# Kernel tuning notes

Measured on AMD Instinct MI355X. Metric: run time of the kernel, lower is better.

## Reference

```python
import jax, jax.numpy as jnp
import numpy as np

N_NODES = 200000
N_EDGES = 1600000
NUM_GRAPHS = 2000
VOCAB = 10000
D = 64
NUM_CLS = 2


def setup_inputs() -> dict:
    key = jax.random.key(0)
    ks = jax.random.split(key, 12)
    x = jax.random.randint(ks[0], (N_NODES,), 0, VOCAB, dtype=jnp.int32)
    edge_index = jax.random.randint(ks[1], (2, N_EDGES), 0, N_NODES, dtype=jnp.int32)
    edge_type = jax.random.randint(ks[2], (N_EDGES,), 0, 8, dtype=jnp.int32)
    batch = jnp.sort(jax.random.randint(ks[3], (N_NODES,), 0, NUM_GRAPHS, dtype=jnp.int32))
    embed_table = jax.random.normal(ks[4], (VOCAB, D), dtype=jnp.float32) * 0.02
    embed_table = embed_table.at[0].set(0.0)  # padding_idx=0
    W1 = jax.random.normal(ks[5], (D, D), dtype=jnp.float32) * (1.0 / np.sqrt(D))
    b1 = jnp.zeros((D,), dtype=jnp.float32)
    W2 = jax.random.normal(ks[6], (D, D), dtype=jnp.float32) * (1.0 / np.sqrt(D))
    b2 = jnp.zeros((D,), dtype=jnp.float32)
    Wlin = jax.random.normal(ks[7], (D, NUM_CLS), dtype=jnp.float32) * (1.0 / np.sqrt(D))
    blin = jnp.zeros((NUM_CLS,), dtype=jnp.float32)
    return {"x": x, "edge_index": edge_index, "edge_type": edge_type, "batch": batch,
            "embed_table": embed_table, "W1": W1, "b1": b1, "W2": W2, "b2": b2,
            "Wlin": Wlin, "blin": blin}


def reference(x, edge_index, edge_type, batch, embed_table, W1, b1, W2, b2, Wlin, blin):
    n = x.shape[0]
    # GCN normalization with self-loops (PyG GCNConv default, edge weight = 1)
    loops = jnp.arange(n, dtype=edge_index.dtype)
    src = jnp.concatenate([edge_index[0], loops])
    dst = jnp.concatenate([edge_index[1], loops])
    deg = jax.ops.segment_sum(jnp.ones_like(src, dtype=jnp.float32), dst, num_segments=n)
    dinv = jax.lax.rsqrt(deg)  # deg >= 1 due to self-loops
    norm = (dinv[src] * dinv[dst])[:, None]  # [E+N, 1]

    def gcn(h, W, b):
        h = h @ W  # transform first (small GEMM)
        agg = jax.ops.segment_sum(norm * h[src], dst, num_segments=n)
        return agg + b

    h = embed_table[x]                      # [N, D] embedding lookup
    h = jax.nn.relu(gcn(h, W1, b1))
    h = jax.nn.relu(gcn(h, W2, b2))
    # global mean pool over graphs
    sums = jax.ops.segment_sum(h, batch, num_segments=NUM_GRAPHS)
    cnts = jax.ops.segment_sum(jnp.ones((n,), dtype=h.dtype), batch, num_segments=NUM_GRAPHS)
    g = sums / jnp.maximum(cnts, 1.0)[:, None]
    return g @ Wlin + blin
```

## Files before the change

### kernel.cpp

```cpp
#include <hip/hip_runtime.h>
#include <hip/hip_fp16.h>


#define DD 64
#define BKT 256
#define MAXK 1024
#define NBLK 256
#define BTE 1024
#define SRCMASK 0x3FFFF
#define PBUF_CAP 4096
#define PCAP 4096
#define CCAP 4880
#define CHCAP 6656

typedef _Float16 half8_t __attribute__((ext_vector_type(8)));
typedef float float4_t __attribute__((ext_vector_type(4)));
union F4H8 { float4 f; half8_t h; };
union H8   { float4 f; __half2 h[4]; };

static __device__ __forceinline__ void atomAddF(float* p, float v) {
    unsafeAtomicAdd(p, v);
}

__global__ __launch_bounds__(256) void prep_kernel(
        const float2* __restrict__ table2, __half2* __restrict__ th2, int n2,
        const float* __restrict__ W1, const float* __restrict__ W2,
        __half* __restrict__ w1t, __half* __restrict__ w2t,
        float* __restrict__ outacc, int G2, int* __restrict__ bcur, int K) {
    int gid = blockIdx.x * 256 + threadIdx.x;
    int stride = gridDim.x * 256;
    for (int i = gid; i < K; i += stride) bcur[i] = i * PCAP;
    for (int i = gid; i < G2; i += stride) outacc[i] = 0.f;
    for (int i = gid; i < n2; i += stride)
        th2[i] = __float22half2_rn(table2[i]);
    for (int i = gid; i < DD * DD; i += stride) {
        int n = i >> 6, k = i & 63;
        w1t[i] = __float2half(W1[k * DD + n]);
        w2t[i] = __float2half(W2[k * DD + n]);
    }
}

__global__ __launch_bounds__(BTE) void fused_fill_kernel(
        const int* __restrict__ src, const int* __restrict__ dst, int E, int CH,
        int* __restrict__ bcur, int* __restrict__ pairbuf, int K) {
    __shared__ int lh[MAXK];
    __shared__ int lpk[CHCAP];
    __shared__ unsigned short lbk[CHCAP];
    int tid = threadIdx.x;
    for (int i = tid; i < K; i += BTE) lh[i] = 0;
    __syncthreads();
    int e0 = blockIdx.x * CH;
    int e1 = min(E, e0 + CH);
    int L = e1 - e0;
    bool fits = (L <= CHCAP);
    if (fits) {
        for (int i = tid; i < L; i += BTE) {
            int s = src[e0 + i], d = dst[e0 + i];
            unsigned b = ((unsigned)d) >> 8;
            lpk[i] = s | ((d & 255) << 24);
            lbk[i] = (unsigned short)b;
            atomicAdd(&lh[b], 1);
        }
    } else {
        for (int e = e0 + tid; e < e1; e += BTE)
            atomicAdd(&lh[((unsigned)dst[e]) >> 8], 1);
    }
    __syncthreads();
    for (int b = tid; b < K; b += BTE) {
        int c = lh[b];
        lh[b] = (c > 0) ? atomicAdd(&bcur[b], c) : 0;
    }
    __syncthreads();
    if (fits) {
        for (int i = tid; i < L; i += BTE) {
            int pos = atomicAdd(&lh[lbk[i]], 1);
            pairbuf[pos] = lpk[i];
        }
    } else {
        for (int e = e0 + tid; e < e1; e += BTE) {
            int s = src[e], d = dst[e];
            int pos = atomicAdd(&lh[((unsigned)d) >> 8], 1);
            pairbuf[pos] = s | ((d & 255) << 24);
        }
    }
}

__global__ __launch_bounds__(256) void build_csr_kernel(
        const int* __restrict__ pairbuf, const int* __restrict__ bcur,
        const int* __restrict__ x, int2* __restrict__ rowinfo,
        float2* __restrict__ xd, __half* __restrict__ dinvh,
        int* __restrict__ csr_src, __half* __restrict__ g1h, int N) {
    __shared__ int cnt[256], basel[256], curl[256];
    __shared__ int pbuf[PBUF_CAP];
    int tid = threadIdx.x;
    int b = blockIdx.x;
    int node0 = b << 8;
    cnt[tid] = 0;
    __syncthreads();
    int bb0 = b * PCAP;
    int L   = bcur[b] - bb0;
    bool fits = (L <= PBUF_CAP);
    if (fits) {
        for (int i = tid; i < L; i += 256) {
            int pk = pairbuf[bb0 + i];
            pbuf[i] = pk;
            atomicAdd(&cnt[((unsigned)pk) >> 24], 1);
        }
    } else {
        for (int i = tid; i < L; i += 256)
            atomicAdd(&cnt[((unsigned)pairbuf[bb0 + i]) >> 24], 1);
    }
    __syncthreads();
    int c  = cnt[tid];
    int pc = (c + 3) & ~3;
    {
        __syncthreads();
        basel[tid] = pc;
        __syncthreads();
        if (tid < 64) {
            int carry = 0;
            for (int cc = 0; cc < 4; ++cc) {
                int orig = basel[cc * 64 + tid];
                int v = orig;
                #pragma unroll
                for (int off = 1; off < 64; off <<= 1) {
                    int t = __shfl_up(v, off);
                    if (tid >= off) v += t;
                }
                int tot = __shfl(v, 63);
                cnt[cc * 64 + tid] = v - orig + carry;
                carry += tot;
            }
        }
        __syncthreads();
    }
    int cb0 = b * CCAP;
    int node = node0 + tid;
    int myBase = cb0 + cnt[tid];
    curl[tid] = myBase;
    if (node < N) {
        rowinfo[node] = make_int2(myBase, pc);
        float di = rsqrtf((float)c + 1.0f);
        xd[node] = make_float2(di, __int_as_float(x[node]));
        dinvh[node] = __float2half(di);
        for (int t = c; t < pc; ++t) csr_src[myBase + t] = N;
    } else if (node == N) {
        xd[N] = make_float2(0.0f, __int_as_float(0));
        dinvh[N] = __float2half(0.0f);
        float2* z = (float2*)(g1h + (size_t)N * DD);
        for (int t = 0; t < DD / 4; ++t) z[t] = make_float2(0.f, 0.f);
    }
    __syncthreads();
    if (fits) {
        for (int i = tid; i < L; i += 256) {
            int pk = pbuf[i];
            int pos = atomicAdd(&curl[((unsigned)pk) >> 24], 1);
            int s = pk & 0x00FFFFFF;
            csr_src[pos] = (int)(((unsigned)s) | (((unsigned)x[s]) << 18));
        }
    } else {
        for (int i = tid; i < L; i += 256) {
            int pk = pairbuf[bb0 + i];
            int pos = atomicAdd(&curl[((unsigned)pk) >> 24], 1);
            int s = pk & 0x00FFFFFF;
            csr_src[pos] = (int)(((unsigned)s) | (((unsigned)x[s]) << 18));
        }
    }
}

#define L1_BODY4(sA)                                                          \
    do {                                                                      \
        unsigned a0 = (unsigned)(sA).x, a1 = (unsigned)(sA).y;                \
        unsigned a2 = (unsigned)(sA).z, a3 = (unsigned)(sA).w;                \
        H8 u0, u1, u2, u3;                                                    \
        u0.f = th4[(size_t)(a0 >> 18) * 8 + j3];                              \
        u1.f = th4[(size_t)(a1 >> 18) * 8 + j3];                              \
        u2.f = th4[(size_t)(a2 >> 18) * 8 + j3];                              \
        u3.f = th4[(size_t)(a3 >> 18) * 8 + j3];                              \
        __half2 w0 = __half2half2(dinvh[a0 & SRCMASK]);                       \
        __half2 w1 = __half2half2(dinvh[a1 & SRCMASK]);                       \
        __half2 w2 = __half2half2(dinvh[a2 & SRCMASK]);                       \
        __half2 w3 = __half2half2(dinvh[a3 & SRCMASK]);                       \
        _Pragma("unroll")                                                     \
        for (int t = 0; t < 4; ++t) {                                         \
            acc0.h[t] = __hfma2(w0, u0.h[t], acc0.h[t]);                      \
            acc1.h[t] = __hfma2(w1, u1.h[t], acc1.h[t]);                      \
            acc2.h[t] = __hfma2(w2, u2.h[t], acc2.h[t]);                      \
            acc3.h[t] = __hfma2(w3, u3.h[t], acc3.h[t]);                      \
        }                                                                     \
    } while (0)

__global__ __launch_bounds__(256, 8) void layer1_kernel(
        const int2* __restrict__ rowinfo,
        const int* __restrict__ csr_src, const float2* __restrict__ xd,
        const __half* __restrict__ dinvh,
        const float4* __restrict__ th4, const __half* __restrict__ wt,
        const float* __restrict__ bias, __half* __restrict__ g1h, int N) {
    __shared__ float4 Hs4[32 * 9];
    __shared__ float dvs[32];
    int row0 = blockIdx.x * 32;
    int tid = threadIdx.x;
    int node_l = tid >> 3, j3 = tid & 7;
    int node = row0 + node_l;
    H8 acc0, acc1, acc2, acc3;
    acc0.f = make_float4(0.f, 0.f, 0.f, 0.f);
    acc1.f = acc0.f; acc2.f = acc0.f; acc3.f = acc0.f;
    __half2 dh = __float2half2_rn(0.f);
    if (node < N) {
        float2 sxd = xd[node];
        float di = sxd.x;
        if (j3 == 0) dvs[node_l] = di;
        dh = __float2half2_rn(di);
        int2 ri = rowinfo[node];
        const int4* cs = (const int4*)(csr_src + ri.x);
        int nq = ri.y >> 2;
        int4 c0 = {0, 0, 0, 0}, c1 = c0, c2 = c0, c3 = c0;
        if (nq > 0) c0 = cs[0];
        if (nq > 1) c1 = cs[1];
        if (nq > 2) c2 = cs[2];
        if (nq > 3) c3 = cs[3];
        H8 tv; tv.f = th4[(size_t)__float_as_int(sxd.y) * 8 + j3];
        acc0.h[0] = __hmul2(dh, tv.h[0]); acc0.h[1] = __hmul2(dh, tv.h[1]);
        acc0.h[2] = __hmul2(dh, tv.h[2]); acc0.h[3] = __hmul2(dh, tv.h[3]);
        if (nq > 0) L1_BODY4(c0);
        if (nq > 1) L1_BODY4(c1);
        if (nq > 2) L1_BODY4(c2);
        if (nq > 3) L1_BODY4(c3);
        for (int q = 4; q < nq; ++q) {
            int4 cq = cs[q];
            L1_BODY4(cq);
        }
        #pragma unroll
        for (int t = 0; t < 4; ++t)
            acc0.h[t] = __hmul2(dh, __hadd2(__hadd2(acc0.h[t], acc1.h[t]),
                                            __hadd2(acc2.h[t], acc3.h[t])));
    }
    Hs4[node_l * 9 + j3] = acc0.f;
    __syncthreads();

    int wave = tid >> 6, lane = tid & 63;
    int m = lane & 15, quad = lane >> 4;
    int ncol = wave * 16 + m;
    F4H8 b0, b1;
    const float4* WT4 = (const float4*)wt;
    b0.f = WT4[ncol * 8 + quad];
    b1.f = WT4[ncol * 8 + 4 + quad];
    float bb_ = bias[ncol];
    #pragma unroll
    for (int t = 0; t < 2; ++t) {
        F4H8 a0, a1;
        a0.f = Hs4[(t * 16 + m) * 9 + quad];
        a1.f = Hs4[(t * 16 + m) * 9 + 4 + quad];
        float4_t acc = {0.f, 0.f, 0.f, 0.f};
        acc = __builtin_amdgcn_mfma_f32_16x16x32_f16(a0.h, b0.h, acc, 0, 0, 0);
        acc = __builtin_amdgcn_mfma_f32_16x16x32_f16(a1.h, b1.h, acc, 0, 0, 0);
        #pragma unroll
        for (int reg = 0; reg < 4; ++reg) {
            int row = t * 16 + quad * 4 + reg;
            int grow = row0 + row;
            if (grow < N) {
                float h = fmaxf(acc[reg] + bb_, 0.0f);
                g1h[(size_t)grow * DD + ncol] = __float2half(dvs[row] * h);
            }
        }
    }
}

#define L2_BODY4(sA)                                                          \
    do {                                                                      \
        H8 u0, u1, u2, u3;                                                    \
        u0.f = g1h4[(size_t)((sA).x & SRCMASK) * 8 + j3];                     \
        u1.f = g1h4[(size_t)((sA).y & SRCMASK) * 8 + j3];                     \
        u2.f = g1h4[(size_t)((sA).z & SRCMASK) * 8 + j3];                     \
        u3.f = g1h4[(size_t)((sA).w & SRCMASK) * 8 + j3];                     \
        _Pragma("unroll")                                                     \
        for (int t = 0; t < 4; ++t) {                                         \
            acc0.h[t] = __hadd2(acc0.h[t], u0.h[t]);                          \
            acc1.h[t] = __hadd2(acc1.h[t], u1.h[t]);                          \
            acc2.h[t] = __hadd2(acc2.h[t], u2.h[t]);                          \
            acc3.h[t] = __hadd2(acc3.h[t], u3.h[t]);                          \
        }                                                                     \
    } while (0)

__global__ __launch_bounds__(256, 8) void layer2_pool_kernel(
        const int2* __restrict__ rowinfo,
        const int* __restrict__ csr_src, const float2* __restrict__ xd,
        const float4* __restrict__ g1h4, const __half* __restrict__ wt,
        const float* __restrict__ bias, const int* __restrict__ batch,
        const float* __restrict__ Wlin, float* __restrict__ outacc, int N) {
    __shared__ float4 Hs4[32 * 9];
    __shared__ float lp0[128], lp1[128];
    __shared__ float p0s[32], p1s[32];
    __shared__ int   bat[32];
    int row0 = blockIdx.x * 32;
    int tid = threadIdx.x;
    int node_l = tid >> 3, j3 = tid & 7;
    int node = row0 + node_l;
    H8 acc0, acc1, acc2, acc3;
    acc0.f = make_float4(0.f, 0.f, 0.f, 0.f);
    acc1.f = acc0.f; acc2.f = acc0.f; acc3.f = acc0.f;
    if (node < N) {
        float di = xd[node].x;
        int2 ri = rowinfo[node];
        const int4* cs = (const int4*)(csr_src + ri.x);
        int nq = ri.y >> 2;
        int4 c0 = {0, 0, 0, 0}, c1 = c0, c2 = c0, c3 = c0;
        if (nq > 0) c0 = cs[0];
        if (nq > 1) c1 = cs[1];
        if (nq > 2) c2 = cs[2];
        if (nq > 3) c3 = cs[3];
        acc0.f = g1h4[(size_t)node * 8 + j3];
        if (nq > 0) L2_BODY4(c0);
        if (nq > 1) L2_BODY4(c1);
        if (nq > 2) L2_BODY4(c2);
        if (nq > 3) L2_BODY4(c3);
        for (int q = 4; q < nq; ++q) {
            int4 cq = cs[q];
            L2_BODY4(cq);
        }
        __half2 dih = __float2half2_rn(di);
        #pragma unroll
        for (int t = 0; t < 4; ++t)
            acc0.h[t] = __hmul2(dih, __hadd2(__hadd2(acc0.h[t], acc1.h[t]),
                                             __hadd2(acc2.h[t], acc3.h[t])));
    }
    Hs4[node_l * 9 + j3] = acc0.f;
    __syncthreads();

    int wave = tid >> 6, lane = tid & 63;
    int m = lane & 15, quad = lane >> 4;
    int ncol = wave * 16 + m;
    F4H8 b0, b1;
    const float4* WT4 = (const float4*)wt;
    b0.f = WT4[ncol * 8 + quad];
    b1.f = WT4[ncol * 8 + 4 + quad];
    float bb_  = bias[ncol];
    float wl0 = Wlin[ncol * 2 + 0];
    float wl1 = Wlin[ncol * 2 + 1];
    #pragma unroll
    for (int t = 0; t < 2; ++t) {
        F4H8 a0, a1;
        a0.f = Hs4[(t * 16 + m) * 9 + quad];
        a1.f = Hs4[(t * 16 + m) * 9 + 4 + quad];
        float4_t acc = {0.f, 0.f, 0.f, 0.f};
        acc = __builtin_amdgcn_mfma_f32_16x16x32_f16(a0.h, b0.h, acc, 0, 0, 0);
        acc = __builtin_amdgcn_mfma_f32_16x16x32_f16(a1.h, b1.h, acc, 0, 0, 0);
        #pragma unroll
        for (int reg = 0; reg < 4; ++reg) {
            int row = t * 16 + quad * 4 + reg;
            int grow = row0 + row;
            float h = (grow < N) ? fmaxf(acc[reg] + bb_, 0.0f) : 0.0f;
            float p0 = h * wl0;
            float p1 = h * wl1;
            #pragma unroll
            for (int off = 8; off >= 1; off >>= 1) {
                p0 += __shfl_xor(p0, off);
                p1 += __shfl_xor(p1, off);
            }
            if (m == 0) {
                lp0[wave * 32 + row] = p0;
                lp1[wave * 32 + row] = p1;
            }
        }
    }
    __syncthreads();
    if (tid < 32) {
        int grow = row0 + tid;
        p0s[tid] = lp0[tid] + lp0[32 + tid] + lp0[64 + tid] + lp0[96 + tid];
        p1s[tid] = lp1[tid] + lp1[32 + tid] + lp1[64 + tid] + lp1[96 + tid];
        bat[tid] = (grow < N) ? batch[grow] : -1;
    }
    __syncthreads();
    if (tid < 32) {
        float s0 = p0s[tid], s1 = p1s[tid];
        int bg = bat[tid];
        #pragma unroll
        for (int off = 1; off < 32; off <<= 1) {
            float t0 = __shfl_down(s0, off);
            float t1 = __shfl_down(s1, off);
            if (tid + off < 32 && bat[tid + off] == bg) {
                s0 += t0;
                s1 += t1;
            }
        }
        bool head = (bg >= 0) && (tid == 0 || bat[tid - 1] != bg);
        if (head) {
            atomAddF(&outacc[bg * 2 + 0], s0);
            atomAddF(&outacc[bg * 2 + 1], s1);
        }
    }
}

__global__ void final_kernel(const float* __restrict__ outacc,
                             const int* __restrict__ batch,
                             const float* __restrict__ blin,
                             float* __restrict__ out, int G, int N) {
    int t = blockIdx.x * blockDim.x + threadIdx.x;
    if (t >= G * 2) return;
    int g = t >> 1, c = t & 1;
    int lo = 0, hi = N;
    while (lo < hi) { int m = (lo + hi) >> 1; if (batch[m] < g) lo = m + 1; else hi = m; }
    int lo2 = lo, hi2 = N;
    while (lo2 < hi2) { int m = (lo2 + hi2) >> 1; if (batch[m] < g + 1) lo2 = m + 1; else hi2 = m; }
    float cnt = (float)(lo2 - lo);
    out[t] = outacc[t] / fmaxf(cnt, 1.0f) + blin[c];
}

extern "C" void kernel_launch(void* const* d_in, const int* in_sizes, int n_in,
                              void* d_out, int out_size, void* d_ws, size_t ws_size,
                              hipStream_t stream) {
    const int*   x      = (const int*)d_in[0];
    const int*   ei     = (const int*)d_in[1];
    const int*   batch  = (const int*)d_in[3];
    const float* table  = (const float*)d_in[4];
    const float* W1     = (const float*)d_in[5];
    const float* b1     = (const float*)d_in[6];
    const float* W2     = (const float*)d_in[7];
    const float* b2     = (const float*)d_in[8];
    const float* Wlin   = (const float*)d_in[9];
    const float* blin   = (const float*)d_in[10];
    float* out = (float*)d_out;

    const int N = in_sizes[0];
    const int E = in_sizes[2];
    const int G = out_size / 2;
    const int TBL = in_sizes[4];

    const int* src = ei;
    const int* dst = ei + E;

    const int K = (N + BKT - 1) / BKT;
    const int CH = (E + NBLK - 1) / NBLK;

    __half* g1h     = (__half*)d_ws;
    __half* th      = g1h + (size_t)(N + 1) * DD;
    __half* w1t     = th + TBL;
    __half* w2t     = w1t + DD * DD;
    int*    pairbuf = (int*)(w2t + DD * DD);
    int*    csr_src = pairbuf + (size_t)K * PCAP;
    int2*   rowinfo = (int2*)(csr_src + (size_t)K * CCAP);
    float2* xd      = (float2*)(rowinfo + N);
    __half* dinvh   = (__half*)(xd + N + 1);
    float*  outacc  = (float*)(dinvh + (size_t)((N + 2) & ~1));
    int*    bcur    = (int*)(outacc + 2 * G);

    const int BT = 256;

    prep_kernel<<<2048, BT, 0, stream>>>((const float2*)table, (__half2*)th,
                                         TBL / 2, W1, W2, w1t, w2t,
                                         outacc, 2 * G, bcur, K);
    fused_fill_kernel<<<NBLK, BTE, 0, stream>>>(src, dst, E, CH, bcur,
                                                pairbuf, K);
    build_csr_kernel<<<K, BT, 0, stream>>>(pairbuf, bcur, x, rowinfo, xd,
                                           dinvh, csr_src, g1h, N);

    int gRow = (N + 31) / 32;
    layer1_kernel<<<gRow, BT, 0, stream>>>(rowinfo, csr_src, xd, dinvh,
                                           (const float4*)th, w1t, b1, g1h, N);
    layer2_pool_kernel<<<gRow, BT, 0, stream>>>(rowinfo, csr_src, xd,
                                                (const float4*)g1h, w2t, b2,
                                                batch, Wlin, outacc, N);
    final_kernel<<<(G * 2 + BT - 1) / BT, BT, 0, stream>>>(outacc, batch, blin,
                                                           out, G, N);
}
```

Before: 204.7 us.

## Renumber nodes within each bucket by degree class to balance aggregation rows

Splits CSR construction into two kernels. The first sorts the nodes of each 256-node bucket by padded-degree class and assigns each a new slot, then writes per-slot row info, degree scales and batch ids. The second places edges using slot-remapped source ids, so rows of similar length sit next to each other and lanes in the layer kernels see less divergence. The pooling segmented scan is rewritten to use the remapped batch array with a flag-based scan, because nodes in a bucket no longer stay sorted by graph. This adds a kernel launch, drops the shared-memory staging of edge pairs, and relies on segments staying correct after the reorder.

```diff
diff --git a/kernel.cpp b/kernel.cpp
--- a/kernel.cpp
+++ b/kernel.cpp
@@ -8,7 +8,6 @@
 #define NBLK 256
 #define BTE 1024
 #define SRCMASK 0x3FFFF
-#define PBUF_CAP 4096
 #define PCAP 4096
 #define CCAP 4880
 #define CHCAP 6656
@@ -85,64 +84,71 @@
     }
 }
 
-__global__ __launch_bounds__(256) void build_csr_kernel(
+__global__ __launch_bounds__(256) void sort_csr_kernel(
         const int* __restrict__ pairbuf, const int* __restrict__ bcur,
-        const int* __restrict__ x, int2* __restrict__ rowinfo,
-        float2* __restrict__ xd, __half* __restrict__ dinvh,
-        int* __restrict__ csr_src, __half* __restrict__ g1h, int N) {
-    __shared__ int cnt[256], basel[256], curl[256];
-    __shared__ int pbuf[PBUF_CAP];
+        const int* __restrict__ x, const int* __restrict__ batch,
+        int2* __restrict__ rowinfo, float2* __restrict__ xd,
+        __half* __restrict__ dinvh, int* __restrict__ slot_x,
+        int* __restrict__ bats, int* __restrict__ csr_src,
+        __half* __restrict__ g1h, int N) {
+    __shared__ int cnt[256], basel[256], sc[256];
+    __shared__ int clscnt[16], clsbase[16];
     int tid = threadIdx.x;
     int b = blockIdx.x;
     int node0 = b << 8;
+    int V = min(256, N - node0);
     cnt[tid] = 0;
+    if (tid < 16) clscnt[tid] = 0;
     __syncthreads();
     int bb0 = b * PCAP;
-    int L   = bcur[b] - bb0;
-    bool fits = (L <= PBUF_CAP);
-    if (fits) {
-        for (int i = tid; i < L; i += 256) {
-            int pk = pairbuf[bb0 + i];
-            pbuf[i] = pk;
-            atomicAdd(&cnt[((unsigned)pk) >> 24], 1);
-        }
-    } else {
-        for (int i = tid; i < L; i += 256)
-            atomicAdd(&cnt[((unsigned)pairbuf[bb0 + i]) >> 24], 1);
-    }
+    int L = bcur[b] - bb0;
+    for (int i = tid; i < L; i += 256)
+        atomicAdd(&cnt[((unsigned)pairbuf[bb0 + i]) >> 24], 1);
     __syncthreads();
     int c  = cnt[tid];
     int pc = (c + 3) & ~3;
-    {
-        __syncthreads();
-        basel[tid] = pc;
-        __syncthreads();
-        if (tid < 64) {
-            int carry = 0;
-            for (int cc = 0; cc < 4; ++cc) {
-                int orig = basel[cc * 64 + tid];
-                int v = orig;
-                #pragma unroll
-                for (int off = 1; off < 64; off <<= 1) {
-                    int t = __shfl_up(v, off);
-                    if (tid >= off) v += t;
-                }
-                int tot = __shfl(v, 63);
-                cnt[cc * 64 + tid] = v - orig + carry;
-                carry += tot;
+    int cls = min(pc >> 2, 15);
+    int intra = 0;
+    if (tid < V) intra = atomicAdd(&clscnt[cls], 1);
+    basel[tid] = 0;
+    __syncthreads();
+    if (tid == 0) {
+        int run = 0;
+        #pragma unroll
+        for (int k = 0; k < 16; ++k) { clsbase[k] = run; run += clscnt[k]; }
+    }
+    __syncthreads();
+    int rank = (tid < V) ? (clsbase[cls] + intra) : 0;
+    if (tid < V) basel[rank] = pc;
+    __syncthreads();
+    if (tid < 64) {
+        int carry = 0;
+        for (int cc = 0; cc < 4; ++cc) {
+            int orig = basel[cc * 64 + tid];
+            int v = orig;
+            #pragma unroll
+            for (int off = 1; off < 64; off <<= 1) {
+                int t = __shfl_up(v, off);
+                if (tid >= off) v += t;
             }
-        }
-        __syncthreads();
-    }
+            int tot = __shfl(v, 63);
+            sc[cc * 64 + tid] = v - orig + carry;
+            carry += tot;
+        }
+    }
+    __syncthreads();
     int cb0 = b * CCAP;
     int node = node0 + tid;
-    int myBase = cb0 + cnt[tid];
-    curl[tid] = myBase;
-    if (node < N) {
-        rowinfo[node] = make_int2(myBase, pc);
+    if (tid < V) {
+        int slot = node0 + rank;
+        int myBase = cb0 + sc[rank];
+        rowinfo[slot] = make_int2(myBase, pc);
         float di = rsqrtf((float)c + 1.0f);
-        xd[node] = make_float2(di, __int_as_float(x[node]));
-        dinvh[node] = __float2half(di);
+        int xv = x[node];
+        xd[slot] = make_float2(di, __int_as_float(xv));
+        dinvh[slot] = __float2half(di);
+        bats[slot] = batch[node];
+        slot_x[node] = slot | (xv << 18);
         for (int t = c; t < pc; ++t) csr_src[myBase + t] = N;
     } else if (node == N) {
         xd[N] = make_float2(0.0f, __int_as_float(0));
@@ -150,21 +156,33 @@
         float2* z = (float2*)(g1h + (size_t)N * DD);
         for (int t = 0; t < DD / 4; ++t) z[t] = make_float2(0.f, 0.f);
     }
-    __syncthreads();
-    if (fits) {
-        for (int i = tid; i < L; i += 256) {
-            int pk = pbuf[i];
-            int pos = atomicAdd(&curl[((unsigned)pk) >> 24], 1);
-            int s = pk & 0x00FFFFFF;
-            csr_src[pos] = (int)(((unsigned)s) | (((unsigned)x[s]) << 18));
-        }
-    } else {
-        for (int i = tid; i < L; i += 256) {
-            int pk = pairbuf[bb0 + i];
-            int pos = atomicAdd(&curl[((unsigned)pk) >> 24], 1);
-            int s = pk & 0x00FFFFFF;
-            csr_src[pos] = (int)(((unsigned)s) | (((unsigned)x[s]) << 18));
-        }
+}
+
+__global__ __launch_bounds__(256) void place_csr_kernel(
+        const int* __restrict__ pairbuf, const int* __restrict__ bcur,
+        const int* __restrict__ slot_x, const int2* __restrict__ rowinfo,
+        int* __restrict__ csr_src, int N) {
+    __shared__ int curl[256];
+    __shared__ unsigned char lrank[256];
+    int tid = threadIdx.x;
+    int b = blockIdx.x;
+    int node0 = b << 8;
+    int V = min(256, N - node0);
+    if (tid < V) {
+        int sx = slot_x[node0 + tid];
+        int rank = (sx & SRCMASK) - node0;
+        lrank[tid] = (unsigned char)rank;
+        curl[rank] = rowinfo[sx & SRCMASK].x;
+    }
+    __syncthreads();
+    int bb0 = b * PCAP;
+    int L = bcur[b] - bb0;
+    for (int i = tid; i < L; i += 256) {
+        int pk = pairbuf[bb0 + i];
+        int loc = ((unsigned)pk) >> 24;
+        int s = pk & 0x00FFFFFF;
+        int pos = atomicAdd(&curl[lrank[loc]], 1);
+        csr_src[pos] = slot_x[s];
     }
 }
 
@@ -286,7 +304,7 @@
         const int2* __restrict__ rowinfo,
         const int* __restrict__ csr_src, const float2* __restrict__ xd,
         const float4* __restrict__ g1h4, const __half* __restrict__ wt,
-        const float* __restrict__ bias, const int* __restrict__ batch,
+        const float* __restrict__ bias, const int* __restrict__ bats,
         const float* __restrict__ Wlin, float* __restrict__ outacc, int N) {
     __shared__ float4 Hs4[32 * 9];
     __shared__ float lp0[128], lp1[128];
@@ -368,19 +386,22 @@
         int grow = row0 + tid;
         p0s[tid] = lp0[tid] + lp0[32 + tid] + lp0[64 + tid] + lp0[96 + tid];
         p1s[tid] = lp1[tid] + lp1[32 + tid] + lp1[64 + tid] + lp1[96 + tid];
-        bat[tid] = (grow < N) ? batch[grow] : -1;
+        bat[tid] = (grow < N) ? bats[grow] : -1;
     }
     __syncthreads();
     if (tid < 32) {
         float s0 = p0s[tid], s1 = p1s[tid];
         int bg = bat[tid];
+        int f = (tid == 31) || (bat[tid + 1] != bg);
         #pragma unroll
         for (int off = 1; off < 32; off <<= 1) {
             float t0 = __shfl_down(s0, off);
             float t1 = __shfl_down(s1, off);
-            if (tid + off < 32 && bat[tid + off] == bg) {
+            int   tf = __shfl_down(f, off);
+            if (tid + off < 32 && !f) {
                 s0 += t0;
                 s1 += t1;
+                f = tf;
             }
         }
         bool head = (bg >= 0) && (tid == 0 || bat[tid - 1] != bg);
@@ -443,6 +464,8 @@
     __half* dinvh   = (__half*)(xd + N + 1);
     float*  outacc  = (float*)(dinvh + (size_t)((N + 2) & ~1));
     int*    bcur    = (int*)(outacc + 2 * G);
+    int*    slot_x  = bcur + K;
+    int*    bats    = slot_x + N;
 
     const int BT = 256;
 
@@ -451,15 +474,18 @@
                                          outacc, 2 * G, bcur, K);
     fused_fill_kernel<<<NBLK, BTE, 0, stream>>>(src, dst, E, CH, bcur,
                                                 pairbuf, K);
-    build_csr_kernel<<<K, BT, 0, stream>>>(pairbuf, bcur, x, rowinfo, xd,
-                                           dinvh, csr_src, g1h, N);
+    sort_csr_kernel<<<K, BT, 0, stream>>>(pairbuf, bcur, x, batch, rowinfo,
+                                          xd, dinvh, slot_x, bats, csr_src,
+                                          g1h, N);
+    place_csr_kernel<<<K, BT, 0, stream>>>(pairbuf, bcur, slot_x, rowinfo,
+                                           csr_src, N);
 
     int gRow = (N + 31) / 32;
     layer1_kernel<<<gRow, BT, 0, stream>>>(rowinfo, csr_src, xd, dinvh,
                                            (const float4*)th, w1t, b1, g1h, N);
     layer2_pool_kernel<<<gRow, BT, 0, stream>>>(rowinfo, csr_src, xd,
                                                 (const float4*)g1h, w2t, b2,
-                                                batch, Wlin, outacc, N);
+                                                bats, Wlin, outacc, N);
     final_kernel<<<(G * 2 + BT - 1) / BT, BT, 0, stream>>>(outacc, batch, blin,
                                                            out, G, N);
 }
```

Result: slower. 219.0 us (+7.0%).
